# Kernel tuning notes

Hardware: AMD Instinct MI355X
Metric: run time of the kernel (lower is better)

## Reference

```python
import jax, jax.numpy as jnp
import numpy as np

B, MAX_NODE, MEM_LEN, DIM, HEADS, LAYERS, DEG = 32, 1024, 256, 128, 4, 4, 16
CH = DIM // HEADS


def setup_inputs() -> dict:
    key = jax.random.key(0)
    ks = jax.random.split(key, 16)
    counts = np.array([512 + 16 * i for i in range(B)])  # ragged graph sizes, sum = 24320
    N = int(counts.sum())
    node2batch = np.repeat(np.arange(B), counts)
    node2pos = np.concatenate([np.arange(c) for c in counts])
    bmask = np.arange(MAX_NODE)[None, :] < counts[:, None]
    rng = np.random.default_rng(0)
    srcs, dsts, off = [], [], 0
    for c in counts:  # edges stay within each graph
        srcs.append(off + rng.integers(0, c, size=DEG * c))
        dsts.append(off + rng.integers(0, c, size=DEG * c))
        off += c
    edge_index = np.stack([np.concatenate(srcs), np.concatenate(dsts)])

    def rn(k, shape, scale=0.05):
        return jax.random.normal(k, shape, jnp.float32) * scale

    return dict(
        node_feats=rn(ks[0], (N, DIM), 1.0),
        edge_feats=rn(ks[1], (edge_index.shape[1], DIM), 1.0),
        memory=rn(ks[2], (B, MEM_LEN, DIM), 1.0),
        Wn=rn(ks[3], (LAYERS, DIM, DIM)), bn=jnp.zeros((LAYERS, DIM)),
        We=rn(ks[4], (LAYERS, DIM, DIM)),
        att_src=rn(ks[5], (LAYERS, HEADS, CH)),
        att_dst=rn(ks[6], (LAYERS, HEADS, CH)),
        att_edge=rn(ks[7], (LAYERS, HEADS, CH)),
        ln1_g=jnp.ones((LAYERS, DIM)), ln1_b=jnp.zeros((LAYERS, DIM)),
        ln2_g=jnp.ones((LAYERS, DIM)), ln2_b=jnp.zeros((LAYERS, DIM)),
        Wq=rn(ks[8], (LAYERS, DIM, DIM)), Wk=rn(ks[9], (LAYERS, DIM, DIM)),
        Wv=rn(ks[10], (LAYERS, DIM, DIM)), Wo=rn(ks[11], (LAYERS, DIM, DIM)),
        Ew1=rn(ks[12], (LAYERS, 3 * DIM, DIM)), Eb1=jnp.zeros((LAYERS, DIM)),
        Ew2=rn(ks[13], (LAYERS, DIM, DIM)), Eb2=jnp.zeros((LAYERS, DIM)),
        edge_index=jnp.asarray(edge_index, jnp.int32),
        node2batch=jnp.asarray(node2batch, jnp.int32),
        node2pos=jnp.asarray(node2pos, jnp.int32),
        batch_mask=jnp.asarray(bmask),
        mem_pad_mask=jnp.ones((B, MEM_LEN), bool),
    )


def _ln(x, g, b):
    mu = x.mean(-1, keepdims=True)
    v = ((x - mu) ** 2).mean(-1, keepdims=True)
    return (x - mu) * jax.lax.rsqrt(v + 1e-5) * g + b


def reference(node_feats, edge_feats, memory, Wn, bn, We, att_src, att_dst, att_edge,
              ln1_g, ln1_b, ln2_g, ln2_b, Wq, Wk, Wv, Wo, Ew1, Eb1, Ew2, Eb2,
              edge_index, node2batch, node2pos, batch_mask, mem_pad_mask):
    N = node_feats.shape[0]
    src, dst = edge_index[0], edge_index[1]
    # [B, max_node, mem_len]: attend only valid memory slots from valid nodes
    cross_mask = mem_pad_mask[:, None, :] & batch_mask[:, :, None]
    x, e = node_feats, edge_feats
    for l in range(LAYERS):
        # --- edge-conditioned GAT conv (segment softmax over dst) ---
        h = (x @ Wn[l]).reshape(N, HEADS, CH)
        eh = (e @ We[l]).reshape(-1, HEADS, CH)
        logits = (h[src] * att_src[l]).sum(-1) + (h[dst] * att_dst[l]).sum(-1) + (eh * att_edge[l]).sum(-1)
        logits = jax.nn.leaky_relu(logits, 0.2)  # [E, H]
        m = jax.ops.segment_max(logits, dst, num_segments=N)
        ew = jnp.exp(logits - m[dst])
        den = jax.ops.segment_sum(ew, dst, num_segments=N)
        alpha = ew / (den[dst] + 1e-16)
        conv = jax.ops.segment_sum(alpha[..., None] * (h[src] + eh), dst, num_segments=N)
        conv = conv.reshape(N, DIM) + bn[l]
        x = jax.nn.relu(_ln(conv, ln1_g[l], ln1_b[l])) + x
        # --- graph2batch scatter into dense padded tensor ---
        dense = jnp.zeros((B, MAX_NODE, DIM), x.dtype).at[node2batch, node2pos].set(x)
        # --- cross attention against memory ---
        q = (dense @ Wq[l]).reshape(B, MAX_NODE, HEADS, CH)
        k = (memory @ Wk[l]).reshape(B, MEM_LEN, HEADS, CH)
        v = (memory @ Wv[l]).reshape(B, MEM_LEN, HEADS, CH)
        scores = jnp.einsum('bqhc,bkhc->bhqk', q, k) / np.float32(np.sqrt(CH))
        scores = jnp.where(cross_mask[:, None], scores, jnp.float32(-1e9))
        ao = jnp.einsum('bhqk,bkhc->bqhc', jax.nn.softmax(scores, axis=-1), v)
        ao = ao.reshape(B, MAX_NODE, DIM) @ Wo[l]
        dense = jax.nn.relu(_ln(ao + dense, ln2_g[l], ln2_b[l]))
        x = dense[node2batch, node2pos]  # batch2graph gather
        # --- residual sparse edge update ---
        ecat = jnp.concatenate([e, x[src], x[dst]], axis=-1)
        e = e + jax.nn.relu(ecat @ Ew1[l] + Eb1[l]) @ Ew2[l] + Eb2[l]
    return x, e
```

## Files before the change

### kernel.cpp

```cpp
#include <hip/hip_runtime.h>

#define DIM    128
#define HEADS  4
#define CH     32
#define MEMLEN 256
#define LAYERS 4


__global__ void copy_f4(const float4* __restrict__ in, float4* __restrict__ out, long n) {
    long i = (long)blockIdx.x * blockDim.x + threadIdx.x;
    long stride = (long)gridDim.x * blockDim.x;
    for (; i < n; i += stride) out[i] = in[i];
}

__global__ void hist_k(const int* __restrict__ dst, int E, int* __restrict__ deg) {
    int e = blockIdx.x * blockDim.x + threadIdx.x;
    if (e < E) atomicAdd(&deg[dst[e]], 1);
}

__global__ void csr_offsets(const int* __restrict__ deg, int n, int* __restrict__ off) {
    __shared__ int part[1024];
    int t = threadIdx.x;
    int chunk = (n + 1023) >> 10;
    int lo = t * chunk, hi = min(lo + chunk, n);
    int s = 0;
    for (int i = lo; i < hi; i++) s += deg[i];
    part[t] = s; __syncthreads();
    for (int d = 1; d < 1024; d <<= 1) {
        int v = part[t];
        int add = (t >= d) ? part[t - d] : 0;
        __syncthreads();
        part[t] = v + add;
        __syncthreads();
    }
    int run = (t == 0) ? 0 : part[t - 1];
    for (int i = lo; i < hi; i++) { off[i] = run; run += deg[i]; }
    if (t == 1023) off[n] = part[1023];
}

__global__ void csr_fill(const int* __restrict__ dst, int E, const int* __restrict__ off,
                         int* __restrict__ cur, int* __restrict__ csr) {
    int e = blockIdx.x * blockDim.x + threadIdx.x;
    if (e < E) {
        int d = dst[e];
        int p = atomicAdd(&cur[d], 1);
        csr[off[d] + p] = e;
    }
}

__global__ __launch_bounds__(256) void gemm128(const float* __restrict__ A,
                                               const float* __restrict__ W,
                                               const float* __restrict__ bias,
                                               float* __restrict__ out, int R) {
    int r0 = blockIdx.x * 64, t = threadIdx.x;
    __shared__ float at[64][DIM];
    for (int i = t; i < 64 * 32; i += 256) {
        int rr = i >> 5, cc = i & 31;
        if (r0 + rr < R)
            ((float4*)at[rr])[cc] = ((const float4*)(A + (size_t)(r0 + rr) * DIM))[cc];
    }
    __syncthreads();
    int c0 = (t & 31) * 4;
    int rb = (t >> 5) * 8;
    float acc[8][4];
#pragma unroll
    for (int ee = 0; ee < 8; ee++)
        acc[ee][0] = acc[ee][1] = acc[ee][2] = acc[ee][3] = 0.f;
    for (int k = 0; k < DIM; k += 4) {
        float4 w0 = *(const float4*)&W[(k + 0) * DIM + c0];
        float4 w1 = *(const float4*)&W[(k + 1) * DIM + c0];
        float4 w2 = *(const float4*)&W[(k + 2) * DIM + c0];
        float4 w3 = *(const float4*)&W[(k + 3) * DIM + c0];
#pragma unroll
        for (int ee = 0; ee < 8; ee++) {
            float4 a = *(float4*)&at[rb + ee][k];
            acc[ee][0] += a.x * w0.x + a.y * w1.x + a.z * w2.x + a.w * w3.x;
            acc[ee][1] += a.x * w0.y + a.y * w1.y + a.z * w2.y + a.w * w3.y;
            acc[ee][2] += a.x * w0.z + a.y * w1.z + a.z * w2.z + a.w * w3.z;
            acc[ee][3] += a.x * w0.w + a.y * w1.w + a.z * w2.w + a.w * w3.w;
        }
    }
    float4 bb = make_float4(0.f, 0.f, 0.f, 0.f);
    if (bias) bb = *(const float4*)&bias[c0];
#pragma unroll
    for (int ee = 0; ee < 8; ee++) {
        int r = r0 + rb + ee;
        if (r < R) {
            float4 o = make_float4(acc[ee][0] + bb.x, acc[ee][1] + bb.y,
                                   acc[ee][2] + bb.z, acc[ee][3] + bb.w);
            *(float4*)&out[(size_t)r * DIM + c0] = o;
        }
    }
}

__global__ __launch_bounds__(256, 2) void gemm128_dual(const float* __restrict__ A,
                                                       const float* __restrict__ Wa,
                                                       const float* __restrict__ Wb,
                                                       const float* __restrict__ biasA,
                                                       float* __restrict__ outA,
                                                       float* __restrict__ outB, int R) {
    int r0 = blockIdx.x * 64, t = threadIdx.x;
    __shared__ float at[64][DIM];
    for (int i = t; i < 64 * 32; i += 256) {
        int rr = i >> 5, cc = i & 31;
        if (r0 + rr < R)
            ((float4*)at[rr])[cc] = ((const float4*)(A + (size_t)(r0 + rr) * DIM))[cc];
    }
    __syncthreads();
    int c0 = (t & 31) * 4;
    int rb = (t >> 5) * 8;
    float accA[8][4], accB[8][4];
#pragma unroll
    for (int ee = 0; ee < 8; ee++)
#pragma unroll
        for (int j = 0; j < 4; j++) { accA[ee][j] = 0.f; accB[ee][j] = 0.f; }
    for (int k = 0; k < DIM; k += 4) {
        float4 wa0 = *(const float4*)&Wa[(k + 0) * DIM + c0];
        float4 wa1 = *(const float4*)&Wa[(k + 1) * DIM + c0];
        float4 wa2 = *(const float4*)&Wa[(k + 2) * DIM + c0];
        float4 wa3 = *(const float4*)&Wa[(k + 3) * DIM + c0];
        float4 wb0 = *(const float4*)&Wb[(k + 0) * DIM + c0];
        float4 wb1 = *(const float4*)&Wb[(k + 1) * DIM + c0];
        float4 wb2 = *(const float4*)&Wb[(k + 2) * DIM + c0];
        float4 wb3 = *(const float4*)&Wb[(k + 3) * DIM + c0];
#pragma unroll
        for (int ee = 0; ee < 8; ee++) {
            float4 a = *(float4*)&at[rb + ee][k];
            accA[ee][0] += a.x * wa0.x + a.y * wa1.x + a.z * wa2.x + a.w * wa3.x;
            accA[ee][1] += a.x * wa0.y + a.y * wa1.y + a.z * wa2.y + a.w * wa3.y;
            accA[ee][2] += a.x * wa0.z + a.y * wa1.z + a.z * wa2.z + a.w * wa3.z;
            accA[ee][3] += a.x * wa0.w + a.y * wa1.w + a.z * wa2.w + a.w * wa3.w;
            accB[ee][0] += a.x * wb0.x + a.y * wb1.x + a.z * wb2.x + a.w * wb3.x;
            accB[ee][1] += a.x * wb0.y + a.y * wb1.y + a.z * wb2.y + a.w * wb3.y;
            accB[ee][2] += a.x * wb0.z + a.y * wb1.z + a.z * wb2.z + a.w * wb3.z;
            accB[ee][3] += a.x * wb0.w + a.y * wb1.w + a.z * wb2.w + a.w * wb3.w;
        }
    }
    float4 bb = make_float4(0.f, 0.f, 0.f, 0.f);
    if (biasA) bb = *(const float4*)&biasA[c0];
#pragma unroll
    for (int ee = 0; ee < 8; ee++) {
        int r = r0 + rb + ee;
        if (r < R) {
            *(float4*)&outA[(size_t)r * DIM + c0] =
                make_float4(accA[ee][0] + bb.x, accA[ee][1] + bb.y,
                            accA[ee][2] + bb.z, accA[ee][3] + bb.w);
            *(float4*)&outB[(size_t)r * DIM + c0] =
                make_float4(accB[ee][0], accB[ee][1], accB[ee][2], accB[ee][3]);
        }
    }
}

__global__ __launch_bounds__(256) void node_proj_tile(
    const float* __restrict__ x, const float* __restrict__ W,
    const float* __restrict__ att_s, const float* __restrict__ att_d,
    float* __restrict__ h, float* __restrict__ ssrc, float* __restrict__ sdst, int N) {
    int r0 = blockIdx.x * 64, t = threadIdx.x;
    __shared__ float at[64][DIM];
    for (int i = t; i < 64 * 32; i += 256) {
        int rr = i >> 5, cc = i & 31;
        if (r0 + rr < N)
            ((float4*)at[rr])[cc] = ((const float4*)(x + (size_t)(r0 + rr) * DIM))[cc];
    }
    __syncthreads();
    int c0 = (t & 31) * 4;
    int rb = (t >> 5) * 8;
    float acc[8][4];
#pragma unroll
    for (int ee = 0; ee < 8; ee++)
        acc[ee][0] = acc[ee][1] = acc[ee][2] = acc[ee][3] = 0.f;
    for (int k = 0; k < DIM; k += 4) {
        float4 w0 = *(const float4*)&W[(k + 0) * DIM + c0];
        float4 w1 = *(const float4*)&W[(k + 1) * DIM + c0];
        float4 w2 = *(const float4*)&W[(k + 2) * DIM + c0];
        float4 w3 = *(const float4*)&W[(k + 3) * DIM + c0];
#pragma unroll
        for (int ee = 0; ee < 8; ee++) {
            float4 a = *(float4*)&at[rb + ee][k];
            acc[ee][0] += a.x * w0.x + a.y * w1.x + a.z * w2.x + a.w * w3.x;
            acc[ee][1] += a.x * w0.y + a.y * w1.y + a.z * w2.y + a.w * w3.y;
            acc[ee][2] += a.x * w0.z + a.y * w1.z + a.z * w2.z + a.w * w3.z;
            acc[ee][3] += a.x * w0.w + a.y * w1.w + a.z * w2.w + a.w * w3.w;
        }
    }
    int hh = (t & 31) >> 3;
    float4 as = *(const float4*)&att_s[c0];
    float4 ad = *(const float4*)&att_d[c0];
#pragma unroll
    for (int ee = 0; ee < 8; ee++) {
        int r = r0 + rb + ee;
        if (r < N) {
            *(float4*)&h[(size_t)r * DIM + c0] =
                make_float4(acc[ee][0], acc[ee][1], acc[ee][2], acc[ee][3]);
            float ps = acc[ee][0]*as.x + acc[ee][1]*as.y + acc[ee][2]*as.z + acc[ee][3]*as.w;
            float pd = acc[ee][0]*ad.x + acc[ee][1]*ad.y + acc[ee][2]*ad.z + acc[ee][3]*ad.w;
#pragma unroll
            for (int mk = 1; mk < 8; mk <<= 1) {
                ps += __shfl_xor(ps, mk, 32);
                pd += __shfl_xor(pd, mk, 32);
            }
            if (((t & 31) & 7) == 0) {
                ssrc[r * HEADS + hh] = ps;
                sdst[r * HEADS + hh] = pd;
            }
        }
    }
}


__global__ void make_waE(const float* __restrict__ We, const float* __restrict__ att_e,
                         float* __restrict__ waE) {
    int k = threadIdx.x;
#pragma unroll
    for (int h = 0; h < HEADS; h++) {
        float s = 0.f;
#pragma unroll
        for (int c = 0; c < CH; c++) s += We[k * DIM + h * CH + c] * att_e[h * CH + c];
        waE[k * HEADS + h] = s;
    }
}

__global__ void sedge_logits(const float* __restrict__ e, const float* __restrict__ waE,
                             const float* __restrict__ ssrc, const float* __restrict__ sdst,
                             const int* __restrict__ src, const int* __restrict__ dst,
                             float* __restrict__ lw, int E) {
    __shared__ float w[DIM * HEADS];
    int t = threadIdx.x;
    w[t] = waE[t]; w[t + 256] = waE[t + 256];
    __syncthreads();
    int g = t >> 5, lane = t & 31;
    int eid = blockIdx.x * 8 + g;
    if (eid >= E) return;
    const float* er = e + (size_t)eid * DIM;
    float s0 = 0.f, s1 = 0.f, s2 = 0.f, s3 = 0.f;
#pragma unroll
    for (int j = 0; j < 4; j++) {
        int k = lane + 32 * j;
        float v = er[k];
        s0 += v * w[k * 4 + 0]; s1 += v * w[k * 4 + 1];
        s2 += v * w[k * 4 + 2]; s3 += v * w[k * 4 + 3];
    }
#pragma unroll
    for (int m = 16; m; m >>= 1) {
        s0 += __shfl_xor(s0, m, 32); s1 += __shfl_xor(s1, m, 32);
        s2 += __shfl_xor(s2, m, 32); s3 += __shfl_xor(s3, m, 32);
    }
    if (lane == 0) {
        int sn = src[eid] * HEADS, dn = dst[eid] * HEADS;
        float l0 = ssrc[sn + 0] + sdst[dn + 0] + s0;
        float l1 = ssrc[sn + 1] + sdst[dn + 1] + s1;
        float l2 = ssrc[sn + 2] + sdst[dn + 2] + s2;
        float l3 = ssrc[sn + 3] + sdst[dn + 3] + s3;
        lw[eid * 4 + 0] = (l0 >= 0.f) ? l0 : 0.2f * l0;
        lw[eid * 4 + 1] = (l1 >= 0.f) ? l1 : 0.2f * l1;
        lw[eid * 4 + 2] = (l2 >= 0.f) ? l2 : 0.2f * l2;
        lw[eid * 4 + 3] = (l3 >= 0.f) ? l3 : 0.2f * l3;
    }
}

__global__ void seg_softmax(const int* __restrict__ off, const int* __restrict__ csr,
                            float* __restrict__ lw, float* __restrict__ den, int NH) {
    int i = blockIdx.x * blockDim.x + threadIdx.x;
    if (i >= NH) return;
    int n = i >> 2, hh = i & 3;
    int o0 = off[n], o1 = off[n + 1];
    float m = -1e30f;
    for (int o = o0; o < o1; o++) m = fmaxf(m, lw[csr[o] * HEADS + hh]);
    float s = 0.f;
    for (int o = o0; o < o1; o++) {
        int idx = csr[o] * HEADS + hh;
        float w = __expf(lw[idx] - m);
        lw[idx] = w;
        s += w;
    }
    den[i] = s;
}

__global__ __launch_bounds__(512) void conv_ln4(
    const int* __restrict__ off, const int* __restrict__ csr, const int* __restrict__ src,
    const float* __restrict__ lw, const float* __restrict__ den,
    const float* __restrict__ hbuf, const float* __restrict__ e, const float* __restrict__ We,
    const float* __restrict__ bn, const float* __restrict__ g, const float* __restrict__ b,
    float* __restrict__ x, int N) {
    int t = threadIdx.x;
    int tt = t & 127, part = t >> 7;
    int n = blockIdx.x;
    int hh = tt >> 5;
    __shared__ float aggeP[4][HEADS][DIM];
    __shared__ float acchP[4][DIM];
    __shared__ float ehcP[4][DIM];
    __shared__ float wred[16];
    int o0 = off[n], o1 = off[n + 1];
    float acch = 0.f, a0 = 0.f, a1 = 0.f, a2 = 0.f, a3 = 0.f;
    for (int o = o0 + part; o < o1; o += 4) {
        int eid = csr[o];
        int s = src[eid];
        float4 al = *(const float4*)&lw[eid * 4];
        acch += ((&al.x)[hh]) * hbuf[(size_t)s * DIM + tt];
        float ev = e[(size_t)eid * DIM + tt];
        a0 += al.x * ev; a1 += al.y * ev; a2 += al.z * ev; a3 += al.w * ev;
    }
    aggeP[part][0][tt] = a0; aggeP[part][1][tt] = a1;
    aggeP[part][2][tt] = a2; aggeP[part][3][tt] = a3;
    acchP[part][tt] = acch;
    __syncthreads();
    float ehc = 0.f;
    int k0 = part * 32;
    for (int k = k0; k < k0 + 32; k++) {
        float ag = aggeP[0][hh][k] + aggeP[1][hh][k] + aggeP[2][hh][k] + aggeP[3][hh][k];
        ehc += ag * We[k * DIM + tt];
    }
    ehcP[part][tt] = ehc;
    __syncthreads();
    float conv = (acchP[0][tt] + acchP[1][tt] + acchP[2][tt] + acchP[3][tt]
                + ehcP[0][tt] + ehcP[1][tt] + ehcP[2][tt] + ehcP[3][tt])
                 / (den[n * HEADS + hh] + 1e-16f) + bn[tt];
    int w = t >> 6;
    float s1 = conv;
#pragma unroll
    for (int mk = 32; mk; mk >>= 1) s1 += __shfl_xor(s1, mk, 64);
    if ((t & 63) == 0) wred[w] = s1;
    __syncthreads();
    float mu = (wred[w] + wred[w ^ 1]) * (1.f / DIM);
    float diff = conv - mu;
    float s2 = diff * diff;
#pragma unroll
    for (int mk = 32; mk; mk >>= 1) s2 += __shfl_xor(s2, mk, 64);
    if ((t & 63) == 0) wred[8 + w] = s2;
    __syncthreads();
    float var = (wred[8 + w] + wred[8 + (w ^ 1)]) * (1.f / DIM);
    if (part == 0) {
        float y = diff * rsqrtf(var + 1e-5f) * g[tt] + b[tt];
        x[(size_t)n * DIM + tt] = fmaxf(y, 0.f) + x[(size_t)n * DIM + tt];
    }
}

__global__ __launch_bounds__(256) void cross_attn_tile(
    float* __restrict__ x, const float* __restrict__ qg,
    const float* __restrict__ kb, const float* __restrict__ vb,
    const float* __restrict__ Wo, const float* __restrict__ g,
    const float* __restrict__ b, const int* __restrict__ boff) {
    int bb = blockIdx.y;
    int n0 = boff[bb] + blockIdx.x * 64;
    int cnt = boff[bb + 1] - n0;
    if (cnt <= 0) return;
    int nq = min(64, cnt);
    int t = threadIdx.x;
    int q = t & 63, h = t >> 6;

    __shared__ float smem[64 * 132];

    float qv[32];
    if (q < nq) {
        const float4* qp = (const float4*)(qg + (size_t)(n0 + q) * DIM + h * CH);
#pragma unroll
        for (int j = 0; j < 8; j++) {
            float4 v = qp[j];
            qv[4*j+0] = v.x; qv[4*j+1] = v.y; qv[4*j+2] = v.z; qv[4*j+3] = v.w;
        }
    } else {
#pragma unroll
        for (int c = 0; c < 32; c++) qv[c] = 0.f;
    }

    float oacc[32];
#pragma unroll
    for (int c = 0; c < 32; c++) oacc[c] = 0.f;
    float m = -1e30f, l = 0.f;

    const float4* Ksrc = (const float4*)(kb + (size_t)bb * MEMLEN * DIM);
    const float4* Vsrc = (const float4*)(vb + (size_t)bb * MEMLEN * DIM);
    float4* Kl = (float4*)smem;
    float4* Vl = (float4*)(smem + 32 * DIM);

    for (int ch = 0; ch < MEMLEN / 32; ch++) {
        __syncthreads();
#pragma unroll
        for (int r = 0; r < 4; r++) {
            int idx = t + r * 256;
            Kl[idx] = Ksrc[ch * 1024 + idx];
            Vl[idx] = Vsrc[ch * 1024 + idx];
        }
        __syncthreads();
        float sc[32];
#pragma unroll
        for (int kk = 0; kk < 32; kk++) {
            const float* kp = smem + kk * DIM + h * CH;
            float s = 0.f;
#pragma unroll
            for (int c = 0; c < 32; c++) s += qv[c] * kp[c];
            sc[kk] = s * 0.17677669529663689f;
        }
        float mc = sc[0];
#pragma unroll
        for (int kk = 1; kk < 32; kk++) mc = fmaxf(mc, sc[kk]);
        float mn = fmaxf(m, mc);
        float scale = __expf(m - mn);
        m = mn;
        float ls = 0.f;
#pragma unroll
        for (int kk = 0; kk < 32; kk++) {
            float w = __expf(sc[kk] - mn);
            sc[kk] = w;
            ls += w;
        }
        l = l * scale + ls;
#pragma unroll
        for (int c = 0; c < 32; c++) oacc[c] *= scale;
#pragma unroll
        for (int kk = 0; kk < 32; kk++) {
            const float* vp = smem + 32 * DIM + kk * DIM + h * CH;
            float w = sc[kk];
#pragma unroll
            for (int c = 0; c < 32; c++) oacc[c] += w * vp[c];
        }
    }
    __syncthreads();
    {
        float inv = 1.f / l;
        float* ap = smem + q * 132 + h * CH;
#pragma unroll
        for (int c = 0; c < 32; c++) ap[c] = oacc[c] * inv;
    }
    __syncthreads();
    int c0 = (t & 31) * 4;
    int rb = (t >> 5) * 8;
    float acc2[8][4];
#pragma unroll
    for (int ee = 0; ee < 8; ee++)
        acc2[ee][0] = acc2[ee][1] = acc2[ee][2] = acc2[ee][3] = 0.f;
    for (int k = 0; k < DIM; k += 4) {
        float4 w0 = *(const float4*)&Wo[(k + 0) * DIM + c0];
        float4 w1 = *(const float4*)&Wo[(k + 1) * DIM + c0];
        float4 w2 = *(const float4*)&Wo[(k + 2) * DIM + c0];
        float4 w3 = *(const float4*)&Wo[(k + 3) * DIM + c0];
#pragma unroll
        for (int ee = 0; ee < 8; ee++) {
            float4 a = *(const float4*)(smem + (rb + ee) * 132 + k);
            acc2[ee][0] += a.x * w0.x + a.y * w1.x + a.z * w2.x + a.w * w3.x;
            acc2[ee][1] += a.x * w0.y + a.y * w1.y + a.z * w2.y + a.w * w3.y;
            acc2[ee][2] += a.x * w0.z + a.y * w1.z + a.z * w2.z + a.w * w3.z;
            acc2[ee][3] += a.x * w0.w + a.y * w1.w + a.z * w2.w + a.w * w3.w;
        }
    }
    float4 gg = *(const float4*)&g[c0];
    float4 bb4 = *(const float4*)&b[c0];
#pragma unroll
    for (int ee = 0; ee < 8; ee++) {
        int r = rb + ee;
        if (r < nq) {
            float4 xr = *(const float4*)&x[(size_t)(n0 + r) * DIM + c0];
            float o0 = acc2[ee][0] + xr.x, o1 = acc2[ee][1] + xr.y;
            float o2 = acc2[ee][2] + xr.z, o3 = acc2[ee][3] + xr.w;
            float s1 = o0 + o1 + o2 + o3;
#pragma unroll
            for (int mk = 16; mk; mk >>= 1) s1 += __shfl_xor(s1, mk, 32);
            float mu = s1 * (1.f / DIM);
            float d0 = o0 - mu, d1 = o1 - mu, d2 = o2 - mu, d3 = o3 - mu;
            float s2 = d0*d0 + d1*d1 + d2*d2 + d3*d3;
#pragma unroll
            for (int mk = 16; mk; mk >>= 1) s2 += __shfl_xor(s2, mk, 32);
            float rs = rsqrtf(s2 * (1.f / DIM) + 1e-5f);
            float4 o = make_float4(fmaxf(d0 * rs * gg.x + bb4.x, 0.f),
                                   fmaxf(d1 * rs * gg.y + bb4.y, 0.f),
                                   fmaxf(d2 * rs * gg.z + bb4.z, 0.f),
                                   fmaxf(d3 * rs * gg.w + bb4.w, 0.f));
            *(float4*)&x[(size_t)(n0 + r) * DIM + c0] = o;
        }
    }
}

__global__ __launch_bounds__(256, 2) void edge_mlp(float* __restrict__ e,
                                                   const float* __restrict__ xs,
                                                   const float* __restrict__ xd,
                                                   const int* __restrict__ src,
                                                   const int* __restrict__ dst,
                                                   const float* __restrict__ W1,
                                                   const float* __restrict__ W2,
                                                   const float* __restrict__ Eb2, int E) {
    int e0 = blockIdx.x * 128, t = threadIdx.x;
    int tx = t & 15, ty = t >> 4;
    int c0 = tx * 8;
    __shared__ float at[128][132];
    for (int i = t; i < 128 * 32; i += 256) {
        int rr = i >> 5, cc = i & 31;
        if (e0 + rr < E)
            *(float4*)&at[rr][cc * 4] = *(const float4*)&e[(size_t)(e0 + rr) * DIM + cc * 4];
    }
    __syncthreads();
    float acc[8][8];
#pragma unroll
    for (int r = 0; r < 8; r++)
#pragma unroll
        for (int c = 0; c < 8; c++) acc[r][c] = 0.f;
    for (int k = 0; k < DIM; k += 4) {
        float4 a4[8];
#pragma unroll
        for (int r = 0; r < 8; r++) a4[r] = *(const float4*)&at[r * 16 + ty][k];
#pragma unroll
        for (int kk = 0; kk < 4; kk++) {
            float4 w0 = *(const float4*)&W1[(size_t)(k + kk) * DIM + c0];
            float4 w1 = *(const float4*)&W1[(size_t)(k + kk) * DIM + c0 + 4];
#pragma unroll
            for (int r = 0; r < 8; r++) {
                float av = (&a4[r].x)[kk];
                acc[r][0] += av * w0.x; acc[r][1] += av * w0.y;
                acc[r][2] += av * w0.z; acc[r][3] += av * w0.w;
                acc[r][4] += av * w1.x; acc[r][5] += av * w1.y;
                acc[r][6] += av * w1.z; acc[r][7] += av * w1.w;
            }
        }
    }
#pragma unroll
    for (int r = 0; r < 8; r++) {
        int row = e0 + r * 16 + ty;
        if (row < E) {
            int sr = src[row], dr = dst[row];
            float4 s0 = *(const float4*)&xs[(size_t)sr * DIM + c0];
            float4 s1 = *(const float4*)&xs[(size_t)sr * DIM + c0 + 4];
            float4 d0 = *(const float4*)&xd[(size_t)dr * DIM + c0];
            float4 d1 = *(const float4*)&xd[(size_t)dr * DIM + c0 + 4];
            acc[r][0] = fmaxf(acc[r][0] + s0.x + d0.x, 0.f);
            acc[r][1] = fmaxf(acc[r][1] + s0.y + d0.y, 0.f);
            acc[r][2] = fmaxf(acc[r][2] + s0.z + d0.z, 0.f);
            acc[r][3] = fmaxf(acc[r][3] + s0.w + d0.w, 0.f);
            acc[r][4] = fmaxf(acc[r][4] + s1.x + d1.x, 0.f);
            acc[r][5] = fmaxf(acc[r][5] + s1.y + d1.y, 0.f);
            acc[r][6] = fmaxf(acc[r][6] + s1.z + d1.z, 0.f);
            acc[r][7] = fmaxf(acc[r][7] + s1.w + d1.w, 0.f);
        }
    }
    __syncthreads();
#pragma unroll
    for (int r = 0; r < 8; r++) {
        *(float4*)&at[r * 16 + ty][c0]     = make_float4(acc[r][0], acc[r][1], acc[r][2], acc[r][3]);
        *(float4*)&at[r * 16 + ty][c0 + 4] = make_float4(acc[r][4], acc[r][5], acc[r][6], acc[r][7]);
    }
    __syncthreads();
#pragma unroll
    for (int r = 0; r < 8; r++)
#pragma unroll
        for (int c = 0; c < 8; c++) acc[r][c] = 0.f;
    for (int k = 0; k < DIM; k += 4) {
        float4 a4[8];
#pragma unroll
        for (int r = 0; r < 8; r++) a4[r] = *(const float4*)&at[r * 16 + ty][k];
#pragma unroll
        for (int kk = 0; kk < 4; kk++) {
            float4 w0 = *(const float4*)&W2[(size_t)(k + kk) * DIM + c0];
            float4 w1 = *(const float4*)&W2[(size_t)(k + kk) * DIM + c0 + 4];
#pragma unroll
            for (int r = 0; r < 8; r++) {
                float av = (&a4[r].x)[kk];
                acc[r][0] += av * w0.x; acc[r][1] += av * w0.y;
                acc[r][2] += av * w0.z; acc[r][3] += av * w0.w;
                acc[r][4] += av * w1.x; acc[r][5] += av * w1.y;
                acc[r][6] += av * w1.z; acc[r][7] += av * w1.w;
            }
        }
    }
    float4 b20 = *(const float4*)&Eb2[c0];
    float4 b21 = *(const float4*)&Eb2[c0 + 4];
#pragma unroll
    for (int r = 0; r < 8; r++) {
        int row = e0 + r * 16 + ty;
        if (row < E) {
            float4 o0 = *(const float4*)&e[(size_t)row * DIM + c0];
            float4 o1 = *(const float4*)&e[(size_t)row * DIM + c0 + 4];
            o0.x += acc[r][0] + b20.x; o0.y += acc[r][1] + b20.y;
            o0.z += acc[r][2] + b20.z; o0.w += acc[r][3] + b20.w;
            o1.x += acc[r][4] + b21.x; o1.y += acc[r][5] + b21.y;
            o1.z += acc[r][6] + b21.z; o1.w += acc[r][7] + b21.w;
            *(float4*)&e[(size_t)row * DIM + c0]     = o0;
            *(float4*)&e[(size_t)row * DIM + c0 + 4] = o1;
        }
    }
}


extern "C" void kernel_launch(void* const* d_in, const int* in_sizes, int n_in,
                              void* d_out, int out_size, void* d_ws, size_t ws_size,
                              hipStream_t stream) {
    const float* node_feats = (const float*)d_in[0];
    const float* edge_feats = (const float*)d_in[1];
    const float* memory     = (const float*)d_in[2];
    const float* Wn   = (const float*)d_in[3];
    const float* bn   = (const float*)d_in[4];
    const float* We   = (const float*)d_in[5];
    const float* att_src  = (const float*)d_in[6];
    const float* att_dst  = (const float*)d_in[7];
    const float* att_edge = (const float*)d_in[8];
    const float* ln1_g = (const float*)d_in[9];
    const float* ln1_b = (const float*)d_in[10];
    const float* ln2_g = (const float*)d_in[11];
    const float* ln2_b = (const float*)d_in[12];
    const float* Wq = (const float*)d_in[13];
    const float* Wk = (const float*)d_in[14];
    const float* Wv = (const float*)d_in[15];
    const float* Wo = (const float*)d_in[16];
    const float* Ew1 = (const float*)d_in[17];
    const float* Eb1 = (const float*)d_in[18];
    const float* Ew2 = (const float*)d_in[19];
    const float* Eb2 = (const float*)d_in[20];
    const int* edge_index = (const int*)d_in[21];
    const int* node2batch = (const int*)d_in[22];

    const int N = in_sizes[0] / DIM;
    const int E = in_sizes[1] / DIM;
    const int Bn = in_sizes[2] / (MEMLEN * DIM);
    const int* srcA = edge_index;
    const int* dstA = edge_index + E;

    float* x = (float*)d_out;
    float* e = x + (size_t)N * DIM;

    char* p = (char*)d_ws;
    auto carve = [&](size_t bytes) {
        void* r = (void*)p;
        p += (bytes + 255) & ~(size_t)255;
        return r;
    };
    float* h     = (float*)carve((size_t)N * DIM * 4);
    float* qg    = (float*)carve((size_t)N * DIM * 4);
    float* xs    = (float*)carve((size_t)N * DIM * 4);
    float* xd    = (float*)carve((size_t)N * DIM * 4);
    float* ssrc  = (float*)carve((size_t)N * HEADS * 4);
    float* sdst  = (float*)carve((size_t)N * HEADS * 4);
    float* lw    = (float*)carve((size_t)E * HEADS * 4);
    float* den   = (float*)carve((size_t)N * HEADS * 4);
    float* waE   = (float*)carve((size_t)DIM * HEADS * 4);
    float* kbuf  = (float*)carve((size_t)Bn * MEMLEN * DIM * 4);
    float* vbuf  = (float*)carve((size_t)Bn * MEMLEN * DIM * 4);
    int* deg     = (int*)carve((size_t)N * 4);
    int* cur     = (int*)carve((size_t)N * 4);
    int* off     = (int*)carve(((size_t)N + 1) * 4);
    int* csr     = (int*)carve((size_t)E * 4);
    int* bcnt    = (int*)carve((size_t)Bn * 4);
    int* boff    = (int*)carve(((size_t)Bn + 1) * 4);

    {
        long nx = (long)N * DIM / 4;
        copy_f4<<<dim3(2048), dim3(256), 0, stream>>>((const float4*)node_feats, (float4*)x, nx);
        long nen = (long)E * DIM / 4;
        copy_f4<<<dim3(4096), dim3(256), 0, stream>>>((const float4*)edge_feats, (float4*)e, nen);
    }

    hipMemsetAsync(deg, 0, (size_t)N * 4, stream);
    hipMemsetAsync(cur, 0, (size_t)N * 4, stream);
    hipMemsetAsync(bcnt, 0, (size_t)Bn * 4, stream);
    hist_k<<<dim3((E + 255) / 256), dim3(256), 0, stream>>>(dstA, E, deg);
    csr_offsets<<<dim3(1), dim3(1024), 0, stream>>>(deg, N, off);
    csr_fill<<<dim3((E + 255) / 256), dim3(256), 0, stream>>>(dstA, E, off, cur, csr);
    hist_k<<<dim3((N + 255) / 256), dim3(256), 0, stream>>>(node2batch, N, bcnt);
    csr_offsets<<<dim3(1), dim3(1024), 0, stream>>>(bcnt, Bn, boff);

    const int mrows = Bn * MEMLEN;
    const int maxTiles = 1024 / 64;
    for (int l = 0; l < LAYERS; l++) {
        const float* Wn_l  = Wn  + (size_t)l * DIM * DIM;
        const float* We_l  = We  + (size_t)l * DIM * DIM;
        const float* Wq_l  = Wq  + (size_t)l * DIM * DIM;
        const float* Wk_l  = Wk  + (size_t)l * DIM * DIM;
        const float* Wv_l  = Wv  + (size_t)l * DIM * DIM;
        const float* Wo_l  = Wo  + (size_t)l * DIM * DIM;
        const float* Ew1_l = Ew1 + (size_t)l * 3 * DIM * DIM;
        const float* Ew2_l = Ew2 + (size_t)l * DIM * DIM;

        node_proj_tile<<<dim3((N + 63) / 64), dim3(256), 0, stream>>>(
            x, Wn_l, att_src + l * DIM, att_dst + l * DIM, h, ssrc, sdst, N);
        make_waE<<<dim3(1), dim3(DIM), 0, stream>>>(We_l, att_edge + l * DIM, waE);
        sedge_logits<<<dim3((E + 7) / 8), dim3(256), 0, stream>>>(
            e, waE, ssrc, sdst, srcA, dstA, lw, E);
        seg_softmax<<<dim3((N * HEADS + 255) / 256), dim3(256), 0, stream>>>(
            off, csr, lw, den, N * HEADS);
        conv_ln4<<<dim3(N), dim3(512), 0, stream>>>(
            off, csr, srcA, lw, den, h, e, We_l,
            bn + l * DIM, ln1_g + l * DIM, ln1_b + l * DIM, x, N);
        gemm128_dual<<<dim3((mrows + 63) / 64), dim3(256), 0, stream>>>(
            memory, Wk_l, Wv_l, nullptr, kbuf, vbuf, mrows);
        gemm128<<<dim3((N + 63) / 64), dim3(256), 0, stream>>>(
            x, Wq_l, nullptr, qg, N);
        cross_attn_tile<<<dim3(maxTiles, Bn), dim3(256), 0, stream>>>(
            x, qg, kbuf, vbuf, Wo_l, ln2_g + l * DIM, ln2_b + l * DIM, boff);
        gemm128_dual<<<dim3((N + 63) / 64), dim3(256), 0, stream>>>(
            x, Ew1_l + (size_t)DIM * DIM, Ew1_l + (size_t)2 * DIM * DIM,
            Eb1 + l * DIM, xs, xd, N);
        edge_mlp<<<dim3((E + 127) / 128), dim3(256), 0, stream>>>(
            e, xs, xd, srcA, dstA, Ew1_l, Ew2_l, Eb2 + l * DIM, E);
    }
}
```

Before: 4.150 ms.

## Run edge MLP on bf16 MFMA with split-precision hi/lo operands

Replaces the FP32 scalar-FMA edge MLP with a kernel built on bf16 MFMA 16x16x32 instructions. Activations and weights are each split into high and low bf16 parts, so the 3-term product keeps close to FP32 accuracy. Weights are pre-converted once per call into transposed bf16 buffers, and activations sit in swizzled LDS. This targets the compute-bound edge GEMMs over about 389K edges per layer, at the cost of three times the MFMA work plus conversion overhead and uncoalesced scalar epilogue loads and stores.

```diff
diff --git a/kernel.cpp b/kernel.cpp
--- a/kernel.cpp
+++ b/kernel.cpp
@@ -5,6 +5,22 @@
 #define CH     32
 #define MEMLEN 256
 #define LAYERS 4
+
+typedef unsigned int uint;
+typedef unsigned short ushort;
+using bf16x8 = __attribute__((ext_vector_type(8))) short;
+using f32x4  = __attribute__((ext_vector_type(4))) float;
+
+__device__ __forceinline__ ushort bf16_rn(float x) {
+    uint u = __float_as_uint(x);
+    uint r = (u + 0x7fffu + ((u >> 16) & 1u)) >> 16;
+    return (ushort)r;
+}
+__device__ __forceinline__ void split_bf(float v, ushort& h, ushort& lo) {
+    h = bf16_rn(v);
+    float hf = __uint_as_float(((uint)h) << 16);
+    lo = bf16_rn(v - hf);
+}
 
 
 __global__ void copy_f4(const float4* __restrict__ in, float4* __restrict__ out, long n) {
@@ -46,6 +62,31 @@
         int p = atomicAdd(&cur[d], 1);
         csr[off[d] + p] = e;
     }
+}
+
+__global__ void make_w1b(const float* __restrict__ Ew1, ushort* __restrict__ W1b) {
+    int i = blockIdx.x * 256 + threadIdx.x;
+    if (i >= LAYERS * 128 * 384) return;
+    int l = i / (128 * 384); int r = i % (128 * 384);
+    int n = r / 384; int k = r % 384;
+    const float* W = Ew1 + (size_t)l * 3 * DIM * DIM;
+    float v = W[(size_t)(k % 128) * DIM + n];
+    ushort h = bf16_rn(v);
+    ushort out = h;
+    if (k >= 256) {
+        float hf = __uint_as_float(((uint)h) << 16);
+        out = bf16_rn(v - hf);
+    }
+    W1b[(size_t)l * 128 * 384 + (size_t)n * 384 + k] = out;
+}
+
+__global__ void make_w2b(const float* __restrict__ Ew2, ushort* __restrict__ W2b) {
+    int i = blockIdx.x * 256 + threadIdx.x;
+    if (i >= LAYERS * 128 * 256) return;
+    int l = i / (128 * 256); int r = i % (128 * 256);
+    int n = r / 256; int k = r % 256;
+    const float* W = Ew2 + (size_t)l * DIM * DIM;
+    W2b[(size_t)l * 128 * 256 + (size_t)n * 256 + k] = bf16_rn(W[(size_t)(k >> 1) * DIM + n]);
 }
 
 __global__ __launch_bounds__(256) void gemm128(const float* __restrict__ A,
@@ -470,109 +511,111 @@
     }
 }
 
-__global__ __launch_bounds__(256, 2) void edge_mlp(float* __restrict__ e,
-                                                   const float* __restrict__ xs,
-                                                   const float* __restrict__ xd,
-                                                   const int* __restrict__ src,
-                                                   const int* __restrict__ dst,
-                                                   const float* __restrict__ W1,
-                                                   const float* __restrict__ W2,
-                                                   const float* __restrict__ Eb2, int E) {
-    int e0 = blockIdx.x * 128, t = threadIdx.x;
-    int tx = t & 15, ty = t >> 4;
-    int c0 = tx * 8;
-    __shared__ float at[128][132];
-    for (int i = t; i < 128 * 32; i += 256) {
-        int rr = i >> 5, cc = i & 31;
-        if (e0 + rr < E)
-            *(float4*)&at[rr][cc * 4] = *(const float4*)&e[(size_t)(e0 + rr) * DIM + cc * 4];
-    }
-    __syncthreads();
-    float acc[8][8];
-#pragma unroll
-    for (int r = 0; r < 8; r++)
-#pragma unroll
-        for (int c = 0; c < 8; c++) acc[r][c] = 0.f;
-    for (int k = 0; k < DIM; k += 4) {
-        float4 a4[8];
-#pragma unroll
-        for (int r = 0; r < 8; r++) a4[r] = *(const float4*)&at[r * 16 + ty][k];
-#pragma unroll
-        for (int kk = 0; kk < 4; kk++) {
-            float4 w0 = *(const float4*)&W1[(size_t)(k + kk) * DIM + c0];
-            float4 w1 = *(const float4*)&W1[(size_t)(k + kk) * DIM + c0 + 4];
-#pragma unroll
-            for (int r = 0; r < 8; r++) {
-                float av = (&a4[r].x)[kk];
-                acc[r][0] += av * w0.x; acc[r][1] += av * w0.y;
-                acc[r][2] += av * w0.z; acc[r][3] += av * w0.w;
-                acc[r][4] += av * w1.x; acc[r][5] += av * w1.y;
-                acc[r][6] += av * w1.z; acc[r][7] += av * w1.w;
+__global__ __launch_bounds__(256) void edge_mlp_mfma(
+    float* __restrict__ e, const float* __restrict__ xs, const float* __restrict__ xd,
+    const int* __restrict__ src, const int* __restrict__ dst,
+    const ushort* __restrict__ W1b,
+    const ushort* __restrict__ W2b,
+    const float* __restrict__ Eb2, int E) {
+    __shared__ ushort As[64 * 256];
+    int t = threadIdx.x;
+    int e0 = blockIdx.x * 64;
+
+#pragma unroll
+    for (int it = 0; it < 8; it++) {
+        int i = t + it * 256;
+        int row = i >> 5, c4 = i & 31;
+        float4 v;
+        if (e0 + row < E) v = *(const float4*)&e[(size_t)(e0 + row) * DIM + c4 * 4];
+        else v = make_float4(0.f, 0.f, 0.f, 0.f);
+        ushort h0, l0, h1, l1, h2, l2, h3, l3;
+        split_bf(v.x, h0, l0); split_bf(v.y, h1, l1);
+        split_bf(v.z, h2, l2); split_bf(v.w, h3, l3);
+        int k = c4 * 4;
+        int off = k & 7;
+        int kbh = (k >> 3) ^ (row & 7);
+        int kbl = ((128 + k) >> 3) ^ (row & 7);
+        uint2 hw, lw2;
+        hw.x = (uint)h0 | ((uint)h1 << 16); hw.y = (uint)h2 | ((uint)h3 << 16);
+        lw2.x = (uint)l0 | ((uint)l1 << 16); lw2.y = (uint)l2 | ((uint)l3 << 16);
+        *(uint2*)&As[row * 256 + kbh * 8 + off] = hw;
+        *(uint2*)&As[row * 256 + kbl * 8 + off] = lw2;
+    }
+    __syncthreads();
+
+    int l = t & 63, wid = t >> 6;
+    int rowbase = wid * 16;
+    int arow = rowbase + (l & 15);
+    int g = l >> 4;
+    int swz = arow & 7;
+
+    f32x4 acc[8];
+#pragma unroll
+    for (int ct = 0; ct < 8; ct++) acc[ct] = (f32x4){0.f, 0.f, 0.f, 0.f};
+
+    for (int ks = 0; ks < 12; ks++) {
+        int ksA = (ks < 8) ? ks : (ks - 8);
+        int kbm = (ksA * 4 + g) ^ swz;
+        bf16x8 af = *(bf16x8*)&As[arow * 256 + kbm * 8];
+#pragma unroll
+        for (int ct = 0; ct < 8; ct++) {
+            int n = (l & 15) + 16 * ct;
+            bf16x8 bf = *(const bf16x8*)&W1b[(size_t)n * 384 + ks * 32 + g * 8];
+            acc[ct] = __builtin_amdgcn_mfma_f32_16x16x32_bf16(af, bf, acc[ct], 0, 0, 0);
+        }
+    }
+
+    int srow[4], drow[4], grow4[4];
+#pragma unroll
+    for (int j = 0; j < 4; j++) {
+        int grow = e0 + rowbase + g * 4 + j;
+        grow4[j] = grow;
+        if (grow < E) { srow[j] = src[grow]; drow[j] = dst[grow]; }
+        else { srow[j] = 0; drow[j] = 0; }
+    }
+#pragma unroll
+    for (int ct = 0; ct < 8; ct++) {
+        int col = (l & 15) + 16 * ct;
+        int kb = col >> 2;
+        int off = (2 * col) & 7;
+#pragma unroll
+        for (int j = 0; j < 4; j++) {
+            float v = acc[ct][j];
+            if (grow4[j] < E)
+                v += xs[(size_t)srow[j] * DIM + col] + xd[(size_t)drow[j] * DIM + col];
+            v = fmaxf(v, 0.f);
+            ushort h, lo;
+            split_bf(v, h, lo);
+            int rowloc = rowbase + g * 4 + j;
+            int kbm = kb ^ (rowloc & 7);
+            *(uint*)&As[rowloc * 256 + kbm * 8 + off] = (uint)h | ((uint)lo << 16);
+        }
+    }
+
+    f32x4 acc2[8];
+#pragma unroll
+    for (int ct = 0; ct < 8; ct++) acc2[ct] = (f32x4){0.f, 0.f, 0.f, 0.f};
+    for (int ks = 0; ks < 8; ks++) {
+        int kbm = (ks * 4 + g) ^ swz;
+        bf16x8 af = *(bf16x8*)&As[arow * 256 + kbm * 8];
+#pragma unroll
+        for (int ct = 0; ct < 8; ct++) {
+            int n = (l & 15) + 16 * ct;
+            bf16x8 bf = *(const bf16x8*)&W2b[(size_t)n * 256 + ks * 32 + g * 8];
+            acc2[ct] = __builtin_amdgcn_mfma_f32_16x16x32_bf16(af, bf, acc2[ct], 0, 0, 0);
+        }
+    }
+
+#pragma unroll
+    for (int ct = 0; ct < 8; ct++) {
+        int col = (l & 15) + 16 * ct;
+        float b2 = Eb2[col];
+#pragma unroll
+        for (int j = 0; j < 4; j++) {
+            if (grow4[j] < E) {
+                size_t idx = (size_t)grow4[j] * DIM + col;
+                e[idx] += acc2[ct][j] + b2;
             }
-        }
-    }
-#pragma unroll
-    for (int r = 0; r < 8; r++) {
-        int row = e0 + r * 16 + ty;
-        if (row < E) {
-            int sr = src[row], dr = dst[row];
-            float4 s0 = *(const float4*)&xs[(size_t)sr * DIM + c0];
-            float4 s1 = *(const float4*)&xs[(size_t)sr * DIM + c0 + 4];
-            float4 d0 = *(const float4*)&xd[(size_t)dr * DIM + c0];
-            float4 d1 = *(const float4*)&xd[(size_t)dr * DIM + c0 + 4];
-            acc[r][0] = fmaxf(acc[r][0] + s0.x + d0.x, 0.f);
-            acc[r][1] = fmaxf(acc[r][1] + s0.y + d0.y, 0.f);
-            acc[r][2] = fmaxf(acc[r][2] + s0.z + d0.z, 0.f);
-            acc[r][3] = fmaxf(acc[r][3] + s0.w + d0.w, 0.f);
-            acc[r][4] = fmaxf(acc[r][4] + s1.x + d1.x, 0.f);
-            acc[r][5] = fmaxf(acc[r][5] + s1.y + d1.y, 0.f);
-            acc[r][6] = fmaxf(acc[r][6] + s1.z + d1.z, 0.f);
-            acc[r][7] = fmaxf(acc[r][7] + s1.w + d1.w, 0.f);
-        }
-    }
-    __syncthreads();
-#pragma unroll
-    for (int r = 0; r < 8; r++) {
-        *(float4*)&at[r * 16 + ty][c0]     = make_float4(acc[r][0], acc[r][1], acc[r][2], acc[r][3]);
-        *(float4*)&at[r * 16 + ty][c0 + 4] = make_float4(acc[r][4], acc[r][5], acc[r][6], acc[r][7]);
-    }
-    __syncthreads();
-#pragma unroll
-    for (int r = 0; r < 8; r++)
-#pragma unroll
-        for (int c = 0; c < 8; c++) acc[r][c] = 0.f;
-    for (int k = 0; k < DIM; k += 4) {
-        float4 a4[8];
-#pragma unroll
-        for (int r = 0; r < 8; r++) a4[r] = *(const float4*)&at[r * 16 + ty][k];
-#pragma unroll
-        for (int kk = 0; kk < 4; kk++) {
-            float4 w0 = *(const float4*)&W2[(size_t)(k + kk) * DIM + c0];
-            float4 w1 = *(const float4*)&W2[(size_t)(k + kk) * DIM + c0 + 4];
-#pragma unroll
-            for (int r = 0; r < 8; r++) {
-                float av = (&a4[r].x)[kk];
-                acc[r][0] += av * w0.x; acc[r][1] += av * w0.y;
-                acc[r][2] += av * w0.z; acc[r][3] += av * w0.w;
-                acc[r][4] += av * w1.x; acc[r][5] += av * w1.y;
-                acc[r][6] += av * w1.z; acc[r][7] += av * w1.w;
-            }
-        }
-    }
-    float4 b20 = *(const float4*)&Eb2[c0];
-    float4 b21 = *(const float4*)&Eb2[c0 + 4];
-#pragma unroll
-    for (int r = 0; r < 8; r++) {
-        int row = e0 + r * 16 + ty;
-        if (row < E) {
-            float4 o0 = *(const float4*)&e[(size_t)row * DIM + c0];
-            float4 o1 = *(const float4*)&e[(size_t)row * DIM + c0 + 4];
-            o0.x += acc[r][0] + b20.x; o0.y += acc[r][1] + b20.y;
-            o0.z += acc[r][2] + b20.z; o0.w += acc[r][3] + b20.w;
-            o1.x += acc[r][4] + b21.x; o1.y += acc[r][5] + b21.y;
-            o1.z += acc[r][6] + b21.z; o1.w += acc[r][7] + b21.w;
-            *(float4*)&e[(size_t)row * DIM + c0]     = o0;
-            *(float4*)&e[(size_t)row * DIM + c0 + 4] = o1;
         }
     }
 }
@@ -631,6 +674,8 @@
     float* waE   = (float*)carve((size_t)DIM * HEADS * 4);
     float* kbuf  = (float*)carve((size_t)Bn * MEMLEN * DIM * 4);
     float* vbuf  = (float*)carve((size_t)Bn * MEMLEN * DIM * 4);
+    ushort* W1b  = (ushort*)carve((size_t)LAYERS * 128 * 384 * 2);
+    ushort* W2b  = (ushort*)carve((size_t)LAYERS * 128 * 256 * 2);
     int* deg     = (int*)carve((size_t)N * 4);
     int* cur     = (int*)carve((size_t)N * 4);
     int* off     = (int*)carve(((size_t)N + 1) * 4);
@@ -644,6 +689,9 @@
         long nen = (long)E * DIM / 4;
         copy_f4<<<dim3(4096), dim3(256), 0, stream>>>((const float4*)edge_feats, (float4*)e, nen);
     }
+
+    make_w1b<<<dim3((LAYERS * 128 * 384 + 255) / 256), dim3(256), 0, stream>>>(Ew1, W1b);
+    make_w2b<<<dim3((LAYERS * 128 * 256 + 255) / 256), dim3(256), 0, stream>>>(Ew2, W2b);
 
     hipMemsetAsync(deg, 0, (size_t)N * 4, stream);
     hipMemsetAsync(cur, 0, (size_t)N * 4, stream);
@@ -660,11 +708,10 @@
         const float* Wn_l  = Wn  + (size_t)l * DIM * DIM;
         const float* We_l  = We  + (size_t)l * DIM * DIM;
         const float* Wq_l  = Wq  + (size_t)l * DIM * DIM;
+        const float* Wo_l  = Wo  + (size_t)l * DIM * DIM;
         const float* Wk_l  = Wk  + (size_t)l * DIM * DIM;
         const float* Wv_l  = Wv  + (size_t)l * DIM * DIM;
-        const float* Wo_l  = Wo  + (size_t)l * DIM * DIM;
         const float* Ew1_l = Ew1 + (size_t)l * 3 * DIM * DIM;
-        const float* Ew2_l = Ew2 + (size_t)l * DIM * DIM;
 
         node_proj_tile<<<dim3((N + 63) / 64), dim3(256), 0, stream>>>(
             x, Wn_l, att_src + l * DIM, att_dst + l * DIM, h, ssrc, sdst, N);
@@ -685,7 +732,9 @@
         gemm128_dual<<<dim3((N + 63) / 64), dim3(256), 0, stream>>>(
             x, Ew1_l + (size_t)DIM * DIM, Ew1_l + (size_t)2 * DIM * DIM,
             Eb1 + l * DIM, xs, xd, N);
-        edge_mlp<<<dim3((E + 127) / 128), dim3(256), 0, stream>>>(
-            e, xs, xd, srcA, dstA, Ew1_l, Ew2_l, Eb2 + l * DIM, E);
-    }
-}
+        edge_mlp_mfma<<<dim3((E + 63) / 64), dim3(256), 0, stream>>>(
+            e, xs, xd, srcA, dstA,
+            W1b + (size_t)l * 128 * 384, W2b + (size_t)l * 128 * 256,
+            Eb2 + l * DIM, E);
+    }
+}
```

New measurement: 4.944 ms. 1.19x slower.
